# Performance work log

Hardware: AMD Instinct MI355X
Metric: run time of the kernel (lower is better)

The kernel has to match this reference:

```python
import jax, jax.numpy as jnp
import numpy as np
from jax import lax

E = 32          # num_experts
H = 1024        # hidden_size
I = 512         # expert intermediate_size
IS = 2048       # shared expert intermediate_size
G = 8           # n_group
TOPK_GROUP = 4
TOP_K = 8
SCALE = 2.5     # routed_scaling_factor
T = 1024        # tokens


def setup_inputs() -> dict:
    key = jax.random.key(0)
    ks = jax.random.split(key, 9)
    s = 0.02
    return {
        "hidden_states": jax.random.normal(ks[0], (T, H), jnp.float32),
        "gate_w": jax.random.normal(ks[1], (E, H), jnp.float32) * s,
        "e_bias": jax.random.normal(ks[2], (E,), jnp.float32) * 0.1,
        "w_gate": jax.random.normal(ks[3], (E, H, I), jnp.float32) * s,
        "w_up": jax.random.normal(ks[4], (E, H, I), jnp.float32) * s,
        "w_down": jax.random.normal(ks[5], (E, I, H), jnp.float32) * s,
        "ws_gate": jax.random.normal(ks[6], (H, IS), jnp.float32) * s,
        "ws_up": jax.random.normal(ks[7], (H, IS), jnp.float32) * s,
        "ws_down": jax.random.normal(ks[8], (IS, H), jnp.float32) * s,
    }


def _routing_combine(logits, e_bias):
    # Deepseekv3RoutingImpl.noaux_tc (non-fused reference path)
    scores = jax.nn.sigmoid(logits)                    # [T, E]
    swb = scores + e_bias                              # [T, E]
    swb_g = swb.reshape(-1, G, E // G)                 # [T, G, E/G]
    group_scores = lax.top_k(swb_g, 2)[0].sum(-1)      # sum of top-2 per group
    _, gidx = lax.top_k(group_scores, TOPK_GROUP)      # [T, TOPK_GROUP]
    gmask = jax.nn.one_hot(gidx, G, dtype=swb.dtype).sum(1)   # [T, G]
    smask = jnp.repeat(gmask, E // G, axis=-1)         # [T, E]
    _, tidx = lax.top_k(swb * smask, TOP_K)            # [T, TOP_K]
    emask = jax.nn.one_hot(tidx, E, dtype=scores.dtype).sum(1)
    sc = scores * emask
    combine = sc / (sc.sum(-1, keepdims=True) + 1e-20) * SCALE
    return combine, tidx


def reference(hidden_states, gate_w, e_bias, w_gate, w_up, w_down, ws_gate, ws_up, ws_down):
    x = hidden_states
    # gate: fp32 logits
    logits = x.astype(jnp.float32) @ gate_w.T          # [T, E]
    combine, _ = _routing_combine(logits, e_bias)
    # routed experts (FusedMoE math): per-expert gated MLP, combined by routing weights
    h1 = jnp.einsum('th,ehi->tei', x, w_gate)          # [T, E, I]
    h2 = jnp.einsum('th,ehi->tei', x, w_up)
    act = jax.nn.silu(h1) * h2
    routed = jnp.einsum('tei,te,eih->th', act, combine.astype(x.dtype), w_down)
    # shared expert GatedMLP
    shared = (jax.nn.silu(x @ ws_gate) * (x @ ws_up)) @ ws_down
    return routed + shared
```

## Files before the change

### kernel.cpp

```cpp
#include <hip/hip_runtime.h>
#include <cstdint>
#include <cmath>

#define T_TOK 1024
#define H_DIM 1024
#define E_NUM 32
#define I_DIM 512
#define IS_DIM 2048
#define NCOL_R 16384
#define NCOL_T 18432
#define SCALE_F 2.5f
#define MAXTILES 96

typedef __bf16 bf16x8 __attribute__((ext_vector_type(8)));
typedef float f32x4 __attribute__((ext_vector_type(4)));

typedef __attribute__((address_space(3))) unsigned int lds_u32_t;
typedef __attribute__((address_space(1))) const unsigned int glb_u32_t;

__device__ __forceinline__ unsigned short f2b(float f) {
    union { float f; uint32_t u; } v; v.f = f;
    return (unsigned short)((v.u + 0x7FFFu + ((v.u >> 16) & 1u)) >> 16);
}

__device__ __forceinline__ void gll16(const unsigned short* g, unsigned short* l) {
    __builtin_amdgcn_global_load_lds((glb_u32_t*)g, (lds_u32_t*)l, 16, 0, 0);
}

__device__ __forceinline__ void routing_wave(const float* __restrict__ x,
                                             const float* __restrict__ gate_w,
                                             const float* __restrict__ e_bias,
                                             float* __restrict__ combine,
                                             int* __restrict__ topk, int t) {
    int l = threadIdx.x & 63;
    int e = l & 31, half = l >> 5;
    const float4* xr = reinterpret_cast<const float4*>(x + (size_t)t * H_DIM + half * 512);
    const float4* wr = reinterpret_cast<const float4*>(gate_w + (size_t)e * H_DIM + half * 512);
    float s = 0.f;
#pragma unroll 8
    for (int j = 0; j < 128; j++) {
        float4 a = xr[j], b = wr[j];
        s += a.x * b.x + a.y * b.y + a.z * b.z + a.w * b.w;
    }
    s += __shfl_xor(s, 32);
    float sg = 1.f / (1.f + expf(-s));
    float swb = sg + e_bias[e];
    float v1 = __shfl_xor(swb, 1), v2 = __shfl_xor(swb, 2), v3 = __shfl_xor(swb, 3);
    float hi01 = fmaxf(swb, v1), lo01 = fminf(swb, v1);
    float hi23 = fmaxf(v2, v3),  lo23 = fminf(v2, v3);
    float gs = fmaxf(hi01, hi23) + fmaxf(fminf(hi01, hi23), fmaxf(lo01, lo23));
    int g = e >> 2;
    int grank = 0;
#pragma unroll
    for (int gg = 0; gg < 8; gg++) {
        float og = __shfl(gs, gg * 4);
        grank += ((og > gs) || (og == gs && gg < g)) ? 1 : 0;
    }
    bool gsel = grank < 4;
    float candv = gsel ? swb : 0.0f;
    int erank = 0;
#pragma unroll
    for (int ee = 0; ee < 32; ee++) {
        float oc = __shfl(candv, ee);
        erank += ((oc > candv) || (oc == candv && ee < e)) ? 1 : 0;
    }
    bool esel = (erank < 8) && (half == 0);
    unsigned long long m = __ballot(esel);
    int idx = __popcll(m & ((1ull << l) - 1ull));
    if (esel) topk[t * 8 + idx] = e;
    float r = esel ? sg : 0.f;
#pragma unroll
    for (int off = 1; off < 64; off <<= 1) r += __shfl_xor(r, off);
    float inv = SCALE_F / (r + 1e-20f);
    if (half == 0) combine[t * E_NUM + e] = esel ? sg * inv : 0.0f;
}

__device__ __forceinline__ void tcvt128_dev(const float* __restrict__ src,
                                            unsigned short* __restrict__ dst,
                                            int C, int DS, int r0, int c0,
                                            float* tbuf) {
    int t = threadIdx.x;
    int lr = t >> 4;
    int c4 = t & 15;
    float4 v0[4], v1[4];
    const float* s0 = src + (size_t)(r0 + lr) * C + c0 + c4 * 4;
#pragma unroll
    for (int p = 0; p < 4; p++) v0[p] = *reinterpret_cast<const float4*>(s0 + (size_t)p * 16 * C);
#pragma unroll
    for (int p = 0; p < 4; p++) v1[p] = *reinterpret_cast<const float4*>(s0 + (size_t)p * 16 * C + 64);
#pragma unroll
    for (int p = 0; p < 4; p++) {
        int row = lr + p * 16;
        int sc4 = (c4 + (row >> 2) + ((row & 3) << 2)) & 15;
        *reinterpret_cast<float4*>(&tbuf[row * 64 + sc4 * 4]) = v0[p];
        *reinterpret_cast<float4*>(&tbuf[4096 + row * 64 + sc4 * 4]) = v1[p];
    }
    __syncthreads();
    int oc = t >> 2, orr = (t & 3) * 16;
    int ob = oc >> 2, off = oc & 3;
#pragma unroll
    for (int half = 0; half < 2; half++) {
        const float* tb = tbuf + half * 4096;
        uint32_t o[8];
#pragma unroll
        for (int j = 0; j < 8; j++) {
            int ra = orr + 2 * j, rb = ra + 1;
            int sa = (ob + (ra >> 2) + ((ra & 3) << 2)) & 15;
            int sb = (ob + (rb >> 2) + ((rb & 3) << 2)) & 15;
            float fa = tb[ra * 64 + sa * 4 + off];
            float fb = tb[rb * 64 + sb * 4 + off];
            o[j] = (uint32_t)f2b(fa) | ((uint32_t)f2b(fb) << 16);
        }
        unsigned short* dp = dst + (size_t)(c0 + half * 64 + oc) * DS + r0 + orr;
        uint4 u0; u0.x = o[0]; u0.y = o[1]; u0.z = o[2]; u0.w = o[3];
        uint4 u1; u1.x = o[4]; u1.y = o[5]; u1.z = o[6]; u1.w = o[7];
        *reinterpret_cast<uint4*>(dp) = u0;
        *reinterpret_cast<uint4*>(dp + 8) = u1;
    }
}

__global__ __launch_bounds__(256)
void prep1_kernel(const float* __restrict__ x, const float* __restrict__ gate_w,
                  const float* __restrict__ e_bias,
                  const float* __restrict__ w_gate, const float* __restrict__ w_up,
                  const float* __restrict__ ws_gate, const float* __restrict__ ws_up,
                  unsigned short* __restrict__ xb, float* __restrict__ combine,
                  int* __restrict__ topk,
                  unsigned short* __restrict__ BG, unsigned short* __restrict__ BU,
                  unsigned short* __restrict__ SG, unsigned short* __restrict__ SU) {
    __shared__ __align__(16) float tbuf[8192];
    int b = blockIdx.x;
    if (b < 1024) {
        int i = b * 256 + threadIdx.x;
        float4 v = reinterpret_cast<const float4*>(x)[i];
        uint2 o;
        o.x = (uint32_t)f2b(v.x) | ((uint32_t)f2b(v.y) << 16);
        o.y = (uint32_t)f2b(v.z) | ((uint32_t)f2b(v.w) << 16);
        reinterpret_cast<uint2*>(xb)[i] = o;
        return;
    }
    b -= 1024;
    if (b < 256) {
        int t = b * 4 + (threadIdx.x >> 6);
        routing_wave(x, gate_w, e_bias, combine, topk, t);
        return;
    }
    b -= 256;
    const float* src; unsigned short* dst; int C, DS, r0, c0;
    if (b < 2048) {
        int batch = b >> 6, q = b & 63;
        src = w_gate + (size_t)batch * 524288; dst = BG + (size_t)batch * 524288;
        C = 512; DS = 1024; r0 = (q >> 2) * 64; c0 = (q & 3) * 128;
    } else if (b < 4096) {
        b -= 2048; int batch = b >> 6, q = b & 63;
        src = w_up + (size_t)batch * 524288; dst = BU + (size_t)batch * 524288;
        C = 512; DS = 1024; r0 = (q >> 2) * 64; c0 = (q & 3) * 128;
    } else if (b < 4352) {
        int q = b - 4096;
        src = ws_gate; dst = SG; C = 2048; DS = 1024; r0 = (q >> 4) * 64; c0 = (q & 15) * 128;
    } else {
        int q = b - 4352;
        src = ws_up; dst = SU; C = 2048; DS = 1024; r0 = (q >> 4) * 64; c0 = (q & 15) * 128;
    }
    tcvt128_dev(src, dst, C, DS, r0, c0, tbuf);
}

__global__ __launch_bounds__(1024)
void listbuild_kernel(const int* __restrict__ topk, int* __restrict__ meta,
                      int* __restrict__ pair_token, int* __restrict__ slot_of) {
    __shared__ int cnt[E_NUM], start[E_NUM], fill[E_NUM];
    int t = threadIdx.x;
    if (t < E_NUM) cnt[t] = 0;
    __syncthreads();
    int ids[8];
#pragma unroll
    for (int r = 0; r < 8; r++) {
        ids[r] = topk[t * 8 + r];
        atomicAdd(&cnt[ids[r]], 1);
    }
    __syncthreads();
    if (t == 0) {
        int acc = 0;
        for (int e = 0; e < E_NUM; e++) {
            int nt = (cnt[e] + 127) >> 7;
            start[e] = acc * 128;
            fill[e] = 0;
            for (int j = 0; j < nt; j++) meta[1 + acc + j] = e;
            acc += nt;
        }
        meta[0] = acc;
    }
    __syncthreads();
    for (int i = t; i < MAXTILES * 128; i += 1024) pair_token[i] = 0;
    __syncthreads();
#pragma unroll
    for (int r = 0; r < 8; r++) {
        int e = ids[r];
        int s = start[e] + atomicAdd(&fill[e], 1);
        pair_token[s] = t;
        slot_of[t * 8 + r] = s;
    }
}

__global__ __launch_bounds__(256, 2)
void gateup_fused(const unsigned short* __restrict__ xb,
                  const unsigned short* __restrict__ BG,
                  const unsigned short* __restrict__ BU,
                  const unsigned short* __restrict__ SG,
                  const unsigned short* __restrict__ SU,
                  const float* __restrict__ combine,
                  const int* __restrict__ pair_token,
                  const int* __restrict__ meta,
                  const float* __restrict__ w_down,
                  const float* __restrict__ ws_down,
                  unsigned short* __restrict__ BDs,
                  unsigned short* __restrict__ BSD,
                  unsigned short* __restrict__ act_s,
                  unsigned short* __restrict__ act_sh) {
    __shared__ __align__(16) unsigned short smem[24576];
    int b = blockIdx.x;
    if (b >= 512) {
        float* tbuf = reinterpret_cast<float*>(smem);
        int bb = b - 512;
        const float* src; unsigned short* dst; int C, DS, r0, c0;
        if (bb < 2048) {
            int batch = bb >> 6, q = bb & 63;
            src = w_down + (size_t)batch * 524288; dst = BDs + (size_t)batch * 524288;
            C = 1024; DS = 512; r0 = (q >> 3) * 64; c0 = (q & 7) * 128;
        } else {
            int q = bb - 2048;
            src = ws_down; dst = BSD; C = 1024; DS = 2048; r0 = (q >> 3) * 64; c0 = (q & 7) * 128;
        }
        tcvt128_dev(src, dst, C, DS, r0, c0, tbuf);
        return;
    }
    bool routed = b < 384;
    int tid = threadIdx.x, lane = tid & 63, w = tid >> 6;
    int wr = w >> 1, wc = w & 1;
    unsigned short* lA  = smem;
    unsigned short* lBg = smem + 8192;
    unsigned short* lBu = smem + 16384;

    int srow = w * 32 + (lane >> 2);
    int schunk = (lane & 3) * 8;
    int aoff = (w * 32) * 32;

    const unsigned short *gA0, *gA1, *gG0, *gU0;
    int e = 0, slot0 = 0, row0 = 0, ci0 = 0;
    if (routed) {
        int tile = b >> 2;
        if (tile >= meta[0]) return;
        e = meta[1 + tile];
        ci0 = (b & 3) * 128;
        slot0 = tile * 128;
        int brow0 = e * I_DIM + ci0;
        int tok0 = pair_token[slot0 + srow];
        int tok1 = pair_token[slot0 + srow + 16];
        gA0 = xb + (size_t)tok0 * H_DIM + schunk;
        gA1 = xb + (size_t)tok1 * H_DIM + schunk;
        gG0 = BG + (size_t)(brow0 + srow) * H_DIM + schunk;
        gU0 = BU + (size_t)(brow0 + srow) * H_DIM + schunk;
    } else {
        int bb = b - 384;
        row0 = (bb >> 4) * 128;
        ci0 = (bb & 15) * 128;
        gA0 = xb + (size_t)(row0 + srow) * H_DIM + schunk;
        gA1 = gA0 + 16 * H_DIM;
        gG0 = SG + (size_t)(ci0 + srow) * H_DIM + schunk;
        gU0 = SU + (size_t)(ci0 + srow) * H_DIM + schunk;
    }

    f32x4 accg[4][4], accu[4][4];
#pragma unroll
    for (int i = 0; i < 4; i++)
#pragma unroll
        for (int j = 0; j < 4; j++)
#pragma unroll
            for (int r = 0; r < 4; r++) { accg[i][j][r] = 0.f; accu[i][j][r] = 0.f; }

#define GU_STAGE(KK, BSEL)                                        \
    do {                                                          \
        int _k0 = (KK) * 32;                                      \
        unsigned short* _a = lA + (BSEL) * 4096 + aoff;           \
        gll16(gA0 + _k0, _a);                                     \
        gll16(gA1 + _k0, _a + 16 * 32);                           \
        unsigned short* _g = lBg + (BSEL) * 4096 + aoff;          \
        gll16(gG0 + _k0, _g);                                     \
        gll16(gG0 + 16 * H_DIM + _k0, _g + 16 * 32);              \
        unsigned short* _u = lBu + (BSEL) * 4096 + aoff;          \
        gll16(gU0 + _k0, _u);                                     \
        gll16(gU0 + 16 * H_DIM + _k0, _u + 16 * 32);              \
    } while (0)

    GU_STAGE(0, 0);
    __syncthreads();
    for (int kk = 0; kk < 32; kk++) {
        int cur = kk & 1;
        if (kk < 31) GU_STAGE(kk + 1, cur ^ 1);
        bf16x8 af[4], bgf[4], buf2[4];
#pragma unroll
        for (int mi = 0; mi < 4; mi++)
            af[mi] = *reinterpret_cast<const bf16x8*>(
                &lA[cur * 4096 + (wr * 64 + mi * 16 + (lane & 15)) * 32 + (lane >> 4) * 8]);
#pragma unroll
        for (int ni = 0; ni < 4; ni++) {
            int nn = cur * 4096 + (wc * 64 + ni * 16 + (lane & 15)) * 32 + (lane >> 4) * 8;
            bgf[ni] = *reinterpret_cast<const bf16x8*>(&lBg[nn]);
            buf2[ni] = *reinterpret_cast<const bf16x8*>(&lBu[nn]);
        }
#pragma unroll
        for (int mi = 0; mi < 4; mi++)
#pragma unroll
            for (int ni = 0; ni < 4; ni++) {
                accg[mi][ni] = __builtin_amdgcn_mfma_f32_16x16x32_bf16(af[mi], bgf[ni], accg[mi][ni], 0, 0, 0);
                accu[mi][ni] = __builtin_amdgcn_mfma_f32_16x16x32_bf16(af[mi], buf2[ni], accu[mi][ni], 0, 0, 0);
            }
        __syncthreads();
    }
#undef GU_STAGE

    int q = lane >> 4, cl = lane & 15;
    if (routed) {
#pragma unroll
        for (int mi = 0; mi < 4; mi++) {
#pragma unroll
            for (int r = 0; r < 4; r++) {
                int row = wr * 64 + mi * 16 + q * 4 + r;
                int token = pair_token[slot0 + row];
                float s = combine[token * E_NUM + e];
#pragma unroll
                for (int ni = 0; ni < 4; ni++) {
                    float g = accg[mi][ni][r], u = accu[mi][ni][r];
                    float a = g / (1.f + expf(-g)) * u * s;
                    act_s[(size_t)(slot0 + row) * I_DIM + ci0 + wc * 64 + ni * 16 + cl] = f2b(a);
                }
            }
        }
    } else {
#pragma unroll
        for (int mi = 0; mi < 4; mi++) {
#pragma unroll
            for (int ni = 0; ni < 4; ni++) {
                int col = ci0 + wc * 64 + ni * 16 + cl;
#pragma unroll
                for (int r = 0; r < 4; r++) {
                    int row = row0 + wr * 64 + mi * 16 + q * 4 + r;
                    float g = accg[mi][ni][r], u = accu[mi][ni][r];
                    float a = g / (1.f + expf(-g)) * u;
                    act_sh[(size_t)row * IS_DIM + col] = f2b(a);
                }
            }
        }
    }
}

__global__ __launch_bounds__(256, 2)
void down_fused(const unsigned short* __restrict__ act_s,
                const unsigned short* __restrict__ BDs,
                const unsigned short* __restrict__ act_sh,
                const unsigned short* __restrict__ BSD,
                const int* __restrict__ meta,
                float* __restrict__ pairpart,
                float* __restrict__ shpart) {
    int b = blockIdx.x;
    bool routed = b < 768;
    int tid = threadIdx.x, lane = tid & 63, w = tid >> 6;
    int wr = w >> 1, wc = w & 1;
    __shared__ __align__(16) unsigned short lA[2][128 * 32];
    __shared__ __align__(16) unsigned short lB[2][128 * 32];

    int srow = w * 32 + (lane >> 2);
    int schunk = (lane & 3) * 8;
    int aoff = (w * 32) * 32;

    const unsigned short *gA0, *gB0;
    size_t ast, bst;
    int kbase, n0, orow;
    float* outp;
    if (routed) {
        int tile = b >> 3;
        if (tile >= meta[0]) return;
        int e = meta[1 + tile];
        n0 = (b & 7) * 128;
        int slot0 = tile * 128;
        gA0 = act_s + (size_t)(slot0 + srow) * I_DIM + schunk;
        gB0 = BDs + (size_t)e * H_DIM * I_DIM + (size_t)(n0 + srow) * I_DIM + schunk;
        ast = I_DIM; bst = I_DIM; kbase = 0;
        outp = pairpart; orow = slot0;
    } else {
        int bb = b - 768;
        int mb = bb >> 5, nb = (bb >> 2) & 7, ks = bb & 3;
        int row0 = mb * 128;
        n0 = nb * 128;
        gA0 = act_sh + (size_t)(row0 + srow) * IS_DIM + schunk;
        gB0 = BSD + (size_t)(n0 + srow) * IS_DIM + schunk;
        ast = IS_DIM; bst = IS_DIM; kbase = ks * 512;
        outp = shpart + ((size_t)ks << 20); orow = row0;
    }

    f32x4 acc[4][4];
#pragma unroll
    for (int i = 0; i < 4; i++)
#pragma unroll
        for (int j = 0; j < 4; j++)
#pragma unroll
            for (int r = 0; r < 4; r++) acc[i][j][r] = 0.f;

#define DN_STAGE(KK, BSEL)                                        \
    do {                                                          \
        size_t _k0 = (size_t)kbase + (size_t)(KK) * 32;           \
        unsigned short* _a = &lA[BSEL][aoff];                     \
        gll16(gA0 + _k0, _a);                                     \
        gll16(gA0 + 16 * ast + _k0, _a + 16 * 32);                \
        unsigned short* _b2 = &lB[BSEL][aoff];                    \
        gll16(gB0 + _k0, _b2);                                    \
        gll16(gB0 + 16 * bst + _k0, _b2 + 16 * 32);               \
    } while (0)

    DN_STAGE(0, 0);
    __syncthreads();
    for (int kk = 0; kk < 16; kk++) {
        int cur = kk & 1;
        if (kk < 15) DN_STAGE(kk + 1, cur ^ 1);
        bf16x8 af[4], bf[4];
#pragma unroll
        for (int mi = 0; mi < 4; mi++)
            af[mi] = *reinterpret_cast<const bf16x8*>(
                &lA[cur][(wr * 64 + mi * 16 + (lane & 15)) * 32 + (lane >> 4) * 8]);
#pragma unroll
        for (int ni = 0; ni < 4; ni++)
            bf[ni] = *reinterpret_cast<const bf16x8*>(
                &lB[cur][(wc * 64 + ni * 16 + (lane & 15)) * 32 + (lane >> 4) * 8]);
#pragma unroll
        for (int mi = 0; mi < 4; mi++)
#pragma unroll
            for (int ni = 0; ni < 4; ni++)
                acc[mi][ni] = __builtin_amdgcn_mfma_f32_16x16x32_bf16(af[mi], bf[ni], acc[mi][ni], 0, 0, 0);
        __syncthreads();
    }
#undef DN_STAGE

    int q = lane >> 4, cl = lane & 15;
#pragma unroll
    for (int mi = 0; mi < 4; mi++) {
#pragma unroll
        for (int ni = 0; ni < 4; ni++) {
            int col = n0 + wc * 64 + ni * 16 + cl;
#pragma unroll
            for (int r = 0; r < 4; r++) {
                int row = orow + wr * 64 + mi * 16 + q * 4 + r;
                outp[(size_t)row * H_DIM + col] = acc[mi][ni][r];
            }
        }
    }
}

__global__ void final_combine(const float* __restrict__ pairpart,
                              const float* __restrict__ shpart,
                              const int* __restrict__ slot_of,
                              float* __restrict__ out) {
    int t = blockIdx.x;
    int h = threadIdx.x * 4;
    float4 o = reinterpret_cast<const float4*>(shpart + (size_t)t * H_DIM + h)[0];
#pragma unroll
    for (int ks = 1; ks < 4; ks++) {
        float4 v = reinterpret_cast<const float4*>(shpart + ((size_t)ks << 20) + (size_t)t * H_DIM + h)[0];
        o.x += v.x; o.y += v.y; o.z += v.z; o.w += v.w;
    }
#pragma unroll
    for (int r = 0; r < 8; r++) {
        int s = slot_of[t * 8 + r];
        float4 v = reinterpret_cast<const float4*>(pairpart + (size_t)s * H_DIM + h)[0];
        o.x += v.x; o.y += v.y; o.z += v.z; o.w += v.w;
    }
    reinterpret_cast<float4*>(out + (size_t)t * H_DIM + h)[0] = o;
}


__global__ void cvt_x_kernel(const float* __restrict__ x, unsigned short* __restrict__ xb) {
    int i = blockIdx.x * 256 + threadIdx.x;
    float4 v = reinterpret_cast<const float4*>(x)[i];
    uint2 o;
    o.x = (uint32_t)f2b(v.x) | ((uint32_t)f2b(v.y) << 16);
    o.y = (uint32_t)f2b(v.z) | ((uint32_t)f2b(v.w) << 16);
    reinterpret_cast<uint2*>(xb)[i] = o;
}

__global__ void routing_kernel(const float* __restrict__ x,
                               const float* __restrict__ gate_w,
                               const float* __restrict__ e_bias,
                               float* __restrict__ combine,
                               int* __restrict__ topk) {
    int t = blockIdx.x;
    routing_wave(x, gate_w, e_bias, combine, topk, t);
}

__global__ __launch_bounds__(256, 2)
void gateup_kernel(const unsigned short* __restrict__ xb,
                   const float* __restrict__ w_gate,
                   const float* __restrict__ w_up,
                   const float* __restrict__ ws_gate,
                   const float* __restrict__ ws_up,
                   const float* __restrict__ combine,
                   unsigned short* __restrict__ act) {
    int mb = blockIdx.x, cb = blockIdx.y;
    int row0 = mb * 128, c0 = cb * 128;
    const float *bg, *bu;
    int bstride, eidx;
    if (c0 < NCOL_R) {
        int e = c0 >> 9, ci = c0 & 511;
        bg = w_gate + (size_t)e * H_DIM * I_DIM + ci;
        bu = w_up   + (size_t)e * H_DIM * I_DIM + ci;
        bstride = I_DIM; eidx = e;
    } else {
        int ci = c0 - NCOL_R;
        bg = ws_gate + ci; bu = ws_up + ci;
        bstride = IS_DIM; eidx = -1;
    }
    __shared__ __align__(16) unsigned short lA[128*32];
    __shared__ __align__(16) unsigned short lBg[128*32];
    __shared__ __align__(16) unsigned short lBu[128*32];
    int tid = threadIdx.x, lane = tid & 63, w = tid >> 6;
    int wr = w >> 1, wc = w & 1;
    f32x4 accg[4][4], accu[4][4];
#pragma unroll
    for (int i = 0; i < 4; i++)
#pragma unroll
        for (int j = 0; j < 4; j++)
#pragma unroll
            for (int r = 0; r < 4; r++) { accg[i][j][r] = 0.f; accu[i][j][r] = 0.f; }
    int ar = tid >> 2, ak = (tid & 3) * 8;
    int bn = tid & 127, bkg = (tid >> 7) * 16;
    for (int kk = 0; kk < H_DIM / 32; kk++) {
        int k0 = kk * 32;
        __syncthreads();
        *reinterpret_cast<uint4*>(&lA[ar*32 + ak]) =
            *reinterpret_cast<const uint4*>(xb + (size_t)(row0 + ar) * H_DIM + k0 + ak);
        *reinterpret_cast<uint4*>(&lA[(ar+64)*32 + ak]) =
            *reinterpret_cast<const uint4*>(xb + (size_t)(row0 + ar + 64) * H_DIM + k0 + ak);
#pragma unroll
        for (int p = 0; p < 4; p++) {
            int kb = bkg + p * 4;
            const float* pg = bg + (size_t)(k0 + kb) * bstride + bn;
            uint2 dg;
            dg.x = (uint32_t)f2b(pg[0])         | ((uint32_t)f2b(pg[bstride])   << 16);
            dg.y = (uint32_t)f2b(pg[2*bstride]) | ((uint32_t)f2b(pg[3*bstride]) << 16);
            *reinterpret_cast<uint2*>(&lBg[bn*32 + kb]) = dg;
            const float* pu = bu + (size_t)(k0 + kb) * bstride + bn;
            uint2 du;
            du.x = (uint32_t)f2b(pu[0])         | ((uint32_t)f2b(pu[bstride])   << 16);
            du.y = (uint32_t)f2b(pu[2*bstride]) | ((uint32_t)f2b(pu[3*bstride]) << 16);
            *reinterpret_cast<uint2*>(&lBu[bn*32 + kb]) = du;
        }
        __syncthreads();
        bf16x8 af[4], bgf[4], buf2[4];
#pragma unroll
        for (int mi = 0; mi < 4; mi++)
            af[mi] = *reinterpret_cast<const bf16x8*>(&lA[(wr*64 + mi*16 + (lane & 15))*32 + (lane >> 4)*8]);
#pragma unroll
        for (int ni = 0; ni < 4; ni++) {
            int nn = (wc*64 + ni*16 + (lane & 15))*32 + (lane >> 4)*8;
            bgf[ni]  = *reinterpret_cast<const bf16x8*>(&lBg[nn]);
            buf2[ni] = *reinterpret_cast<const bf16x8*>(&lBu[nn]);
        }
#pragma unroll
        for (int mi = 0; mi < 4; mi++)
#pragma unroll
            for (int ni = 0; ni < 4; ni++) {
                accg[mi][ni] = __builtin_amdgcn_mfma_f32_16x16x32_bf16(af[mi], bgf[ni],  accg[mi][ni], 0, 0, 0);
                accu[mi][ni] = __builtin_amdgcn_mfma_f32_16x16x32_bf16(af[mi], buf2[ni], accu[mi][ni], 0, 0, 0);
            }
    }
    int q = lane >> 4, cl = lane & 15;
#pragma unroll
    for (int mi = 0; mi < 4; mi++) {
#pragma unroll
        for (int ni = 0; ni < 4; ni++) {
            int colg = c0 + wc*64 + ni*16 + cl;
#pragma unroll
            for (int r = 0; r < 4; r++) {
                int row = row0 + wr*64 + mi*16 + q*4 + r;
                float g = accg[mi][ni][r], u = accu[mi][ni][r];
                float a = g / (1.f + expf(-g)) * u;
                float s = (eidx >= 0) ? combine[row * E_NUM + eidx] : 1.0f;
                act[(size_t)row * NCOL_T + colg] = f2b(a * s);
            }
        }
    }
}

__global__ __launch_bounds__(256, 2)
void down_kernel(const unsigned short* __restrict__ act,
                 const float* __restrict__ w_down,
                 const float* __restrict__ ws_down,
                 float* __restrict__ partials) {
    int mb = blockIdx.x, nb = blockIdx.y, ks = blockIdx.z;
    int row0 = mb * 128, n0 = nb * 128;
    __shared__ __align__(16) unsigned short lA[128*32];
    __shared__ __align__(16) unsigned short lB[128*32];
    int tid = threadIdx.x, lane = tid & 63, w = tid >> 6;
    int wr = w >> 1, wc = w & 1;
    f32x4 acc[4][4];
#pragma unroll
    for (int i = 0; i < 4; i++)
#pragma unroll
        for (int j = 0; j < 4; j++)
#pragma unroll
            for (int r = 0; r < 4; r++) acc[i][j][r] = 0.f;
    int ar = tid >> 2, ak = (tid & 3) * 8;
    int bn = tid & 127, bkg = (tid >> 7) * 16;
    for (int kk = 0; kk < 144; kk++) {
        int k0 = ks * 4608 + kk * 32;
        const float* bb = (k0 < NCOL_R) ? (w_down + (size_t)k0 * H_DIM)
                                        : (ws_down + (size_t)(k0 - NCOL_R) * H_DIM);
        __syncthreads();
        *reinterpret_cast<uint4*>(&lA[ar*32 + ak]) =
            *reinterpret_cast<const uint4*>(act + (size_t)(row0 + ar) * NCOL_T + k0 + ak);
        *reinterpret_cast<uint4*>(&lA[(ar+64)*32 + ak]) =
            *reinterpret_cast<const uint4*>(act + (size_t)(row0 + ar + 64) * NCOL_T + k0 + ak);
#pragma unroll
        for (int p = 0; p < 4; p++) {
            int kb = bkg + p * 4;
            const float* pb = bb + (size_t)kb * H_DIM + n0 + bn;
            uint2 d;
            d.x = (uint32_t)f2b(pb[0])       | ((uint32_t)f2b(pb[H_DIM])   << 16);
            d.y = (uint32_t)f2b(pb[2*H_DIM]) | ((uint32_t)f2b(pb[3*H_DIM]) << 16);
            *reinterpret_cast<uint2*>(&lB[bn*32 + kb]) = d;
        }
        __syncthreads();
        bf16x8 af[4], bf[4];
#pragma unroll
        for (int mi = 0; mi < 4; mi++)
            af[mi] = *reinterpret_cast<const bf16x8*>(&lA[(wr*64 + mi*16 + (lane & 15))*32 + (lane >> 4)*8]);
#pragma unroll
        for (int ni = 0; ni < 4; ni++)
            bf[ni] = *reinterpret_cast<const bf16x8*>(&lB[(wc*64 + ni*16 + (lane & 15))*32 + (lane >> 4)*8]);
#pragma unroll
        for (int mi = 0; mi < 4; mi++)
#pragma unroll
            for (int ni = 0; ni < 4; ni++)
                acc[mi][ni] = __builtin_amdgcn_mfma_f32_16x16x32_bf16(af[mi], bf[ni], acc[mi][ni], 0, 0, 0);
    }
    float* pout = partials + ((size_t)ks << 20);
    int q = lane >> 4, cl = lane & 15;
#pragma unroll
    for (int mi = 0; mi < 4; mi++) {
#pragma unroll
        for (int ni = 0; ni < 4; ni++) {
            int col = n0 + wc*64 + ni*16 + cl;
#pragma unroll
            for (int r = 0; r < 4; r++) {
                int row = row0 + wr*64 + mi*16 + q*4 + r;
                pout[(size_t)row * H_DIM + col] = acc[mi][ni][r];
            }
        }
    }
}

__global__ void reduce_kernel(const float* __restrict__ p, float* __restrict__ out) {
    int i = blockIdx.x * 256 + threadIdx.x;
    float4 a = reinterpret_cast<const float4*>(p)[i];
    float4 b = reinterpret_cast<const float4*>(p + (size_t)1048576)[i];
    float4 c = reinterpret_cast<const float4*>(p + (size_t)2097152)[i];
    float4 d = reinterpret_cast<const float4*>(p + (size_t)3145728)[i];
    float4 o;
    o.x = a.x + b.x + c.x + d.x;
    o.y = a.y + b.y + c.y + d.y;
    o.z = a.z + b.z + c.z + d.z;
    o.w = a.w + b.w + c.w + d.w;
    reinterpret_cast<float4*>(out)[i] = o;
}

extern "C" void kernel_launch(void* const* d_in, const int* in_sizes, int n_in,
                              void* d_out, int out_size, void* d_ws, size_t ws_size,
                              hipStream_t stream) {
    const float* x       = (const float*)d_in[0];
    const float* gate_w  = (const float*)d_in[1];
    const float* e_bias  = (const float*)d_in[2];
    const float* w_gate  = (const float*)d_in[3];
    const float* w_up    = (const float*)d_in[4];
    const float* w_down  = (const float*)d_in[5];
    const float* ws_gate = (const float*)d_in[6];
    const float* ws_up   = (const float*)d_in[7];
    const float* ws_down = (const float*)d_in[8];
    float* out = (float*)d_out;

    char* ws = (char*)d_ws;
    bool fast = ws_size >= 170000384ull;

    if (fast) {
        float* combine      = (float*)(ws);
        int*   topk         = (int*)(ws + 131072);
        int*   meta         = (int*)(ws + 163840);
        int*   pair_token   = (int*)(ws + 164352);
        int*   slot_of      = (int*)(ws + 213504);
        unsigned short* xb  = (unsigned short*)(ws + 262144);
        unsigned short* act_s  = (unsigned short*)(ws + 2359296);
        unsigned short* act_sh = (unsigned short*)(ws + 14942208);
        unsigned short* BG  = (unsigned short*)(ws + 19136512);
        unsigned short* BU  = (unsigned short*)(ws + 52690944);
        unsigned short* SG  = (unsigned short*)(ws + 86245376);
        unsigned short* SU  = (unsigned short*)(ws + 90439680);
        unsigned short* BDs = (unsigned short*)(ws + 94633984);
        unsigned short* BSD = (unsigned short*)(ws + 128188416);
        float* pairpart     = (float*)(ws + 19136512);
        float* shpart       = (float*)(ws + 69468160);

        prep1_kernel<<<5888, 256, 0, stream>>>(x, gate_w, e_bias, w_gate, w_up,
                                               ws_gate, ws_up,
                                               xb, combine, topk, BG, BU, SG, SU);
        listbuild_kernel<<<1, 1024, 0, stream>>>(topk, meta, pair_token, slot_of);
        gateup_fused<<<2816, 256, 0, stream>>>(xb, BG, BU, SG, SU, combine, pair_token, meta,
                                               w_down, ws_down, BDs, BSD, act_s, act_sh);
        down_fused<<<1024, 256, 0, stream>>>(act_s, BDs, act_sh, BSD, meta, pairpart, shpart);
        final_combine<<<1024, 256, 0, stream>>>(pairpart, shpart, slot_of, out);
    } else {
        float* combine     = (float*)(ws);
        int*   topk        = (int*)(ws + 131072);
        unsigned short* xb = (unsigned short*)(ws + 262144);
        unsigned short* act= (unsigned short*)(ws + 2359296);
        float* partials    = (float*)(ws + 40108032);

        cvt_x_kernel<<<1024, 256, 0, stream>>>(x, xb);
        routing_kernel<<<1024, 64, 0, stream>>>(x, gate_w, e_bias, combine, topk);
        gateup_kernel<<<dim3(8, 144), 256, 0, stream>>>(xb, w_gate, w_up, ws_gate, ws_up, combine, act);
        down_kernel<<<dim3(8, 8, 4), 256, 0, stream>>>(act, w_down, ws_down, partials);
        reduce_kernel<<<1024, 256, 0, stream>>>(partials, out);
    }
}
```

Baseline: 338.7 us.

## Convert weight transposes per-wave with 32x64 tiles and loop over tiles

```diff
diff --git a/kernel.cpp b/kernel.cpp
--- a/kernel.cpp
+++ b/kernel.cpp
@@ -75,48 +75,40 @@
     if (half == 0) combine[t * E_NUM + e] = esel ? sg * inv : 0.0f;
 }
 
-__device__ __forceinline__ void tcvt128_dev(const float* __restrict__ src,
-                                            unsigned short* __restrict__ dst,
-                                            int C, int DS, int r0, int c0,
-                                            float* tbuf) {
-    int t = threadIdx.x;
-    int lr = t >> 4;
-    int c4 = t & 15;
-    float4 v0[4], v1[4];
-    const float* s0 = src + (size_t)(r0 + lr) * C + c0 + c4 * 4;
-#pragma unroll
-    for (int p = 0; p < 4; p++) v0[p] = *reinterpret_cast<const float4*>(s0 + (size_t)p * 16 * C);
-#pragma unroll
-    for (int p = 0; p < 4; p++) v1[p] = *reinterpret_cast<const float4*>(s0 + (size_t)p * 16 * C + 64);
-#pragma unroll
-    for (int p = 0; p < 4; p++) {
-        int row = lr + p * 16;
-        int sc4 = (c4 + (row >> 2) + ((row & 3) << 2)) & 15;
-        *reinterpret_cast<float4*>(&tbuf[row * 64 + sc4 * 4]) = v0[p];
-        *reinterpret_cast<float4*>(&tbuf[4096 + row * 64 + sc4 * 4]) = v1[p];
-    }
-    __syncthreads();
-    int oc = t >> 2, orr = (t & 3) * 16;
-    int ob = oc >> 2, off = oc & 3;
-#pragma unroll
-    for (int half = 0; half < 2; half++) {
-        const float* tb = tbuf + half * 4096;
-        uint32_t o[8];
-#pragma unroll
-        for (int j = 0; j < 8; j++) {
-            int ra = orr + 2 * j, rb = ra + 1;
-            int sa = (ob + (ra >> 2) + ((ra & 3) << 2)) & 15;
-            int sb = (ob + (rb >> 2) + ((rb & 3) << 2)) & 15;
-            float fa = tb[ra * 64 + sa * 4 + off];
-            float fb = tb[rb * 64 + sb * 4 + off];
-            o[j] = (uint32_t)f2b(fa) | ((uint32_t)f2b(fb) << 16);
-        }
-        unsigned short* dp = dst + (size_t)(c0 + half * 64 + oc) * DS + r0 + orr;
-        uint4 u0; u0.x = o[0]; u0.y = o[1]; u0.z = o[2]; u0.w = o[3];
-        uint4 u1; u1.x = o[4]; u1.y = o[5]; u1.z = o[6]; u1.w = o[7];
-        *reinterpret_cast<uint4*>(dp) = u0;
-        *reinterpret_cast<uint4*>(dp + 8) = u1;
-    }
+__device__ __forceinline__ void tcvt_wave(const float* __restrict__ src,
+                                          unsigned short* __restrict__ dst,
+                                          int C, int DS, int r0, int c0,
+                                          float* wt) {
+    int l = threadIdx.x & 63;
+    int lr = l >> 2, c4 = l & 3;
+    uint32_t up[2][8];
+#pragma unroll
+    for (int pass = 0; pass < 2; pass++) {
+        const float* s0 = src + (size_t)(r0 + pass * 16 + lr) * C + c0 + c4 * 4;
+        float4 v[4];
+#pragma unroll
+        for (int p = 0; p < 4; p++)
+            v[p] = *reinterpret_cast<const float4*>(s0 + p * 16);
+#pragma unroll
+        for (int p = 0; p < 4; p++)
+            *reinterpret_cast<float4*>(&wt[lr * 68 + c4 * 4 + p * 16]) = v[p];
+        float w[16];
+#pragma unroll
+        for (int r = 0; r < 16; r++) w[r] = wt[r * 68 + l];
+#pragma unroll
+        for (int j = 0; j < 8; j++)
+            up[pass][j] = (uint32_t)f2b(w[2 * j]) | ((uint32_t)f2b(w[2 * j + 1]) << 16);
+    }
+    unsigned short* dp = dst + (size_t)(c0 + l) * DS + r0;
+    uint4 u;
+    u.x = up[0][0]; u.y = up[0][1]; u.z = up[0][2]; u.w = up[0][3];
+    *reinterpret_cast<uint4*>(dp) = u;
+    u.x = up[0][4]; u.y = up[0][5]; u.z = up[0][6]; u.w = up[0][7];
+    *reinterpret_cast<uint4*>(dp + 8) = u;
+    u.x = up[1][0]; u.y = up[1][1]; u.z = up[1][2]; u.w = up[1][3];
+    *reinterpret_cast<uint4*>(dp + 16) = u;
+    u.x = up[1][4]; u.y = up[1][5]; u.z = up[1][6]; u.w = up[1][7];
+    *reinterpret_cast<uint4*>(dp + 24) = u;
 }
 
 __global__ __launch_bounds__(256)
@@ -128,41 +120,49 @@
                   int* __restrict__ topk,
                   unsigned short* __restrict__ BG, unsigned short* __restrict__ BU,
                   unsigned short* __restrict__ SG, unsigned short* __restrict__ SU) {
-    __shared__ __align__(16) float tbuf[8192];
+    __shared__ __align__(16) float tbuf[4][1088];
     int b = blockIdx.x;
-    if (b < 1024) {
-        int i = b * 256 + threadIdx.x;
-        float4 v = reinterpret_cast<const float4*>(x)[i];
-        uint2 o;
-        o.x = (uint32_t)f2b(v.x) | ((uint32_t)f2b(v.y) << 16);
-        o.y = (uint32_t)f2b(v.z) | ((uint32_t)f2b(v.w) << 16);
-        reinterpret_cast<uint2*>(xb)[i] = o;
-        return;
-    }
-    b -= 1024;
     if (b < 256) {
         int t = b * 4 + (threadIdx.x >> 6);
         routing_wave(x, gate_w, e_bias, combine, topk, t);
         return;
     }
-    b -= 256;
-    const float* src; unsigned short* dst; int C, DS, r0, c0;
-    if (b < 2048) {
-        int batch = b >> 6, q = b & 63;
-        src = w_gate + (size_t)batch * 524288; dst = BG + (size_t)batch * 524288;
-        C = 512; DS = 1024; r0 = (q >> 2) * 64; c0 = (q & 3) * 128;
-    } else if (b < 4096) {
-        b -= 2048; int batch = b >> 6, q = b & 63;
-        src = w_up + (size_t)batch * 524288; dst = BU + (size_t)batch * 524288;
-        C = 512; DS = 1024; r0 = (q >> 2) * 64; c0 = (q & 3) * 128;
-    } else if (b < 4352) {
-        int q = b - 4096;
-        src = ws_gate; dst = SG; C = 2048; DS = 1024; r0 = (q >> 4) * 64; c0 = (q & 15) * 128;
-    } else {
-        int q = b - 4352;
-        src = ws_up; dst = SU; C = 2048; DS = 1024; r0 = (q >> 4) * 64; c0 = (q & 15) * 128;
-    }
-    tcvt128_dev(src, dst, C, DS, r0, c0, tbuf);
+    if (b < 512) {
+        int bb = b - 256;
+#pragma unroll
+        for (int p = 0; p < 4; p++) {
+            int i = bb * 1024 + p * 256 + threadIdx.x;
+            float4 v = reinterpret_cast<const float4*>(x)[i];
+            uint2 o;
+            o.x = (uint32_t)f2b(v.x) | ((uint32_t)f2b(v.y) << 16);
+            o.y = (uint32_t)f2b(v.z) | ((uint32_t)f2b(v.w) << 16);
+            reinterpret_cast<uint2*>(xb)[i] = o;
+        }
+        return;
+    }
+    int wid = (b - 512) * 4 + (threadIdx.x >> 6);
+    float* wt = tbuf[threadIdx.x >> 6];
+#pragma unroll 1
+    for (int s = 0; s < 3; s++) {
+        int t = wid * 3 + s;
+        const float* src; unsigned short* dst; int C, tr, tc;
+        if (t < 8192) {
+            int e = t >> 8, rem = t & 255;
+            src = w_gate + (size_t)e * 524288; dst = BG + (size_t)e * 524288;
+            C = 512; tr = rem & 31; tc = rem >> 5;
+        } else if (t < 16384) {
+            int tt = t - 8192; int e = tt >> 8, rem = tt & 255;
+            src = w_up + (size_t)e * 524288; dst = BU + (size_t)e * 524288;
+            C = 512; tr = rem & 31; tc = rem >> 5;
+        } else if (t < 17408) {
+            int rem = t - 16384;
+            src = ws_gate; dst = SG; C = 2048; tr = rem & 31; tc = rem >> 5;
+        } else {
+            int rem = t - 17408;
+            src = ws_up; dst = SU; C = 2048; tr = rem & 31; tc = rem >> 5;
+        }
+        tcvt_wave(src, dst, C, 1024, tr * 32, tc * 64, wt);
+    }
 }
 
 __global__ __launch_bounds__(1024)
@@ -220,18 +220,22 @@
     __shared__ __align__(16) unsigned short smem[24576];
     int b = blockIdx.x;
     if (b >= 512) {
-        float* tbuf = reinterpret_cast<float*>(smem);
-        int bb = b - 512;
-        const float* src; unsigned short* dst; int C, DS, r0, c0;
-        if (bb < 2048) {
-            int batch = bb >> 6, q = bb & 63;
-            src = w_down + (size_t)batch * 524288; dst = BDs + (size_t)batch * 524288;
-            C = 1024; DS = 512; r0 = (q >> 3) * 64; c0 = (q & 7) * 128;
-        } else {
-            int q = bb - 2048;
-            src = ws_down; dst = BSD; C = 1024; DS = 2048; r0 = (q >> 3) * 64; c0 = (q & 7) * 128;
-        }
-        tcvt128_dev(src, dst, C, DS, r0, c0, tbuf);
+        float* wt = reinterpret_cast<float*>(smem) + (threadIdx.x >> 6) * 1088;
+        int wid = (b - 512) * 4 + (threadIdx.x >> 6);
+#pragma unroll 1
+        for (int s = 0; s < 3; s++) {
+            int t = wid * 3 + s;
+            const float* src; unsigned short* dst; int C, DS, tr, tc;
+            if (t < 8192) {
+                int e = t >> 8, rem = t & 255;
+                src = w_down + (size_t)e * 524288; dst = BDs + (size_t)e * 524288;
+                C = 1024; DS = 512; tr = rem & 15; tc = rem >> 4;
+            } else {
+                int rem = t - 8192;
+                src = ws_down; dst = BSD; C = 1024; DS = 2048; tr = rem & 63; tc = rem >> 6;
+            }
+            tcvt_wave(src, dst, C, DS, tr * 32, tc * 64, wt);
+        }
         return;
     }
     bool routed = b < 384;
@@ -706,11 +710,11 @@
         float* pairpart     = (float*)(ws + 19136512);
         float* shpart       = (float*)(ws + 69468160);
 
-        prep1_kernel<<<5888, 256, 0, stream>>>(x, gate_w, e_bias, w_gate, w_up,
+        prep1_kernel<<<2048, 256, 0, stream>>>(x, gate_w, e_bias, w_gate, w_up,
                                                ws_gate, ws_up,
                                                xb, combine, topk, BG, BU, SG, SU);
         listbuild_kernel<<<1, 1024, 0, stream>>>(topk, meta, pair_token, slot_of);
-        gateup_fused<<<2816, 256, 0, stream>>>(xb, BG, BU, SG, SU, combine, pair_token, meta,
+        gateup_fused<<<1280, 256, 0, stream>>>(xb, BG, BU, SG, SU, combine, pair_token, meta,
                                                w_down, ws_down, BDs, BSD, act_s, act_sh);
         down_fused<<<1024, 256, 0, stream>>>(act_s, BDs, act_sh, BSD, meta, pairpart, shpart);
         final_combine<<<1024, 256, 0, stream>>>(pairpart, shpart, slot_of, out);
```

New measurement: 371.5 us. 9.7% more time.
